# Kernel tuning notes

Measured on AMD Instinct MI355X. Metric: run time of the kernel, lower is better.

Reference implementation:

```python
import jax, jax.numpy as jnp
import numpy as np

HIDDEN = 768
NUM_HEADS = 12
HEAD_DIM = HIDDEN // NUM_HEADS
WINDOW = 128
NEG = -1e30  # stand-in for -inf that is safe under autodiff


def setup_inputs() -> dict:
    key = jax.random.key(0)
    ks = jax.random.split(key, 12)
    B, S = 2, 2048
    hidden = jax.random.normal(ks[0], (B, S, HIDDEN), dtype=jnp.float32)
    attention_mask = jnp.ones((B, S), dtype=jnp.int32)
    global_mask = jax.random.randint(ks[1], (B, S), 0, 2, dtype=jnp.int32)
    def lin(kw, kb):
        W = jax.random.normal(kw, (HIDDEN, HIDDEN), dtype=jnp.float32) * 0.02
        b = jax.random.normal(kb, (HIDDEN,), dtype=jnp.float32) * 0.02
        return W, b
    Wq, bq = lin(ks[2], ks[3])
    Wk, bk = lin(ks[4], ks[5])
    Wv, bv = lin(ks[6], ks[7])
    Wo, bo = lin(ks[8], ks[9])
    return {"hidden": hidden, "attention_mask": attention_mask, "global_mask": global_mask,
            "Wq": Wq, "bq": bq, "Wk": Wk, "bk": bk, "Wv": Wv, "bv": bv, "Wo": Wo, "bo": bo}


def _attend(hidden, attention_mask, global_mask, Wq, bq, Wk, bk, Wv, bv, Wo, bo):
    B, S, H = hidden.shape
    def proj(W, b):
        # (B,S,H) -> (B,nh,S,hd); nn.Linear computes x @ W.T + b
        return (hidden @ W.T + b).reshape(B, S, NUM_HEADS, HEAD_DIM).transpose(0, 2, 1, 3)
    q, k, v = proj(Wq, bq), proj(Wk, bk), proj(Wv, bv)
    scale = jnp.asarray(np.sqrt(HEAD_DIM), dtype=hidden.dtype)
    scores = jnp.einsum('bhqd,bhkd->bhqk', q, k) / scale  # (B,nh,S,S)
    # sliding window mask: |i-j| <= WINDOW
    idx = jnp.arange(S)
    window = (jnp.abs(idx[:, None] - idx[None, :]) <= WINDOW)  # (S,S)
    g = global_mask.astype(bool)
    combined = window[None] | g[:, :, None] | g[:, None, :]     # (B,S,S)
    combined = combined & attention_mask.astype(bool)[:, None, :]  # pad mask on keys
    scores = jnp.where(combined[:, None, :, :], scores, NEG)
    attn = jax.nn.softmax(scores, axis=-1)
    # torch code zeroes NaN rows (fully masked); replicate safely
    attn = jnp.where(jnp.isnan(attn), 0.0, attn)
    out = jnp.einsum('bhqk,bhkd->bhqd', attn, v)  # (B,nh,S,hd)
    out = out.transpose(0, 2, 1, 3).reshape(B, S, H)
    return out @ Wo.T + bo


def reference(hidden, attention_mask, global_mask, Wq, bq, Wk, bk, Wv, bv, Wo, bo):
    return _attend(hidden, attention_mask, global_mask, Wq, bq, Wk, bk, Wv, bv, Wo, bo)
```

## Files before the change

### kernel.cpp

```cpp
#include <hip/hip_runtime.h>
#include <math.h>

#define S_LEN 2048
#define HID   768
#define NH    12
#define HD    64
#define WIN   128
#define NEGV  (-1e30f)
#define QSCALE 0.1803368801111204f
#define MCONST 12.0f
#define NROW  49152

typedef __attribute__((ext_vector_type(8))) short short8v;
typedef __attribute__((ext_vector_type(16))) float f32x16;
typedef unsigned short u16;

__device__ __forceinline__ u16 f2bf(float f) {
    union { float f; unsigned int u; } c; c.f = f;
    unsigned int u = c.u + 0x7FFFu + ((c.u >> 16) & 1u);
    return (u16)(u >> 16);
}

__device__ __forceinline__ short8v cvt8(float4 a, float4 b) {
    short8v t;
    t[0]=(short)f2bf(a.x); t[1]=(short)f2bf(a.y); t[2]=(short)f2bf(a.z); t[3]=(short)f2bf(a.w);
    t[4]=(short)f2bf(b.x); t[5]=(short)f2bf(b.y); t[6]=(short)f2bf(b.z); t[7]=(short)f2bf(b.w);
    return t;
}

__device__ __forceinline__ unsigned int pk2bf(float a, float b) {
    unsigned int r;
    asm("v_cvt_pk_bf16_f32 %0, %1, %2" : "=v"(r) : "v"(a), "v"(b));
    return r;
}

__device__ __forceinline__ float exp2_fast(float x) {
    float r;
    asm("v_exp_f32 %0, %1" : "=v"(r) : "v"(x));
    return r;
}

__device__ __forceinline__ float bf2f(u16 v) {
    union { float f; unsigned u; } c; c.u = ((unsigned)v) << 16; return c.f;
}

__device__ __forceinline__ void gload_lds16(const void* g, void* l) {
    __builtin_amdgcn_global_load_lds(
        (const __attribute__((address_space(1))) unsigned int*)g,
        (__attribute__((address_space(3))) unsigned int*)l, 16, 0, 0);
}

__device__ __forceinline__ void cinit_uni(f32x16& S, const float* src) {
    #pragma unroll
    for (int m = 0; m < 4; m++) {
        float4 f = *(const float4*)(src + 8*m);
        S[4*m+0]=f.x; S[4*m+1]=f.y; S[4*m+2]=f.z; S[4*m+3]=f.w;
    }
}
__device__ __forceinline__ void cinit_mixed(f32x16& S, const float* fa, const float* fb,
                                            int ebase, int gq) {
    #pragma unroll
    for (int m = 0; m < 4; m++) {
        float4 a = *(const float4*)(fa + 8*m);
        float4 b = *(const float4*)(fb + 8*m);
        const int e = ebase - 8*m;
        S[4*m+0] = (gq || (unsigned)(e     + 128) <= 256u) ? a.x : b.x;
        S[4*m+1] = (gq || (unsigned)(e - 1 + 128) <= 256u) ? a.y : b.y;
        S[4*m+2] = (gq || (unsigned)(e - 2 + 128) <= 256u) ? a.z : b.z;
        S[4*m+3] = (gq || (unsigned)(e - 3 + 128) <= 256u) ? a.w : b.w;
    }
}

__global__ __launch_bounds__(256) void convert_inputs(
    const float* __restrict__ hidden, const float* __restrict__ Wq,
    const float* __restrict__ Wk, const float* __restrict__ Wv,
    const float* __restrict__ Wo, const int* __restrict__ amask,
    const int* __restrict__ gmask, u16* __restrict__ hbf,
    u16* __restrict__ w4, float* __restrict__ fAg, float* __restrict__ fBg)
{
    const int y = blockIdx.y;
    if (y == 5) {
        const int idx = (blockIdx.x*256 + threadIdx.x) * 8;
        if (idx >= 2*S_LEN) return;
        #pragma unroll
        for (int u = 0; u < 8; u++) {
            const int am = amask[idx+u], gk = gmask[idx+u];
            fAg[idx+u] = am ? -MCONST : NEGV;
            fBg[idx+u] = (am && gk) ? -MCONST : NEGV;
        }
        return;
    }
    const float* src; u16* dst; int n; float scale = 1.f;
    if (y == 0) { src = hidden; dst = hbf; n = 4096*HID; }
    else {
        src = (y==1) ? Wq : (y==2) ? Wk : (y==3) ? Wv : Wo;
        dst = w4 + (size_t)(y-1)*HID*HID;
        n = HID*HID;
        if (y == 1) scale = QSCALE;
    }
    const int idx = (blockIdx.x*256 + threadIdx.x) * 8;
    if (idx >= n) return;
    float4 f0 = *(const float4*)(src + idx);
    float4 f1 = *(const float4*)(src + idx + 4);
    f0.x*=scale; f0.y*=scale; f0.z*=scale; f0.w*=scale;
    f1.x*=scale; f1.y*=scale; f1.z*=scale; f1.w*=scale;
    *(short8v*)(dst + idx) = cvt8(f0, f1);
}

typedef __attribute__((ext_vector_type(4))) float float4v;
__global__ __launch_bounds__(256) void gemm_mfma(
    const u16* __restrict__ A, const u16* __restrict__ W4,
    const float* __restrict__ bA, const float* __restrict__ bB,
    const float* __restrict__ bC, u16* __restrict__ obf,
    u16* __restrict__ ovt, float* __restrict__ of32, int mode)
{
    __shared__ __align__(16) u16 As[128*32];
    __shared__ __align__(16) u16 Bs[128*32];

    const int tid = threadIdx.x;
    const int w = tid >> 6, l = tid & 63;
    const int lx = l & 15, lg = l >> 4;
    const int wr = w >> 1, wc = w & 1;
    const int m0 = blockIdx.x * 128, n0 = blockIdx.y * 128;
    const int z = (mode == 0) ? blockIdx.z : 3;
    const float* bias = (mode == 1) ? bA : (z == 0 ? bA : (z == 1 ? bB : bC));
    const float bscale = (mode == 0 && z == 0) ? QSCALE : 1.0f;
    const u16* Wp = W4 + (size_t)z * (HID*HID);

    float4v acc[4][4];
    const float4v fz = {0.f,0.f,0.f,0.f};
    #pragma unroll
    for (int i = 0; i < 4; i++)
        #pragma unroll
        for (int j = 0; j < 4; j++) acc[i][j] = fz;

    for (int kt = 0; kt < HID/32; kt++) {
        const int k0 = kt * 32;
        __syncthreads();
        #pragma unroll
        for (int rnd = 0; rnd < 2; rnd++) {
            const int ch  = rnd*256 + w*64 + l;
            const int row = ch >> 2, kc = ch & 3;
            gload_lds16(A  + (size_t)(m0+row)*HID + k0 + kc*8,
                        As + (size_t)(rnd*256 + w*64)*8);
            gload_lds16(Wp + (size_t)(n0+row)*HID + k0 + kc*8,
                        Bs + (size_t)(rnd*256 + w*64)*8);
        }
        __syncthreads();
        short8v af[4], bfr[4];
        #pragma unroll
        for (int i = 0; i < 4; i++) {
            af[i]  = *(const short8v*)(As + (wr*64 + i*16 + lx)*32 + lg*8);
            bfr[i] = *(const short8v*)(Bs + (wc*64 + i*16 + lx)*32 + lg*8);
        }
        #pragma unroll
        for (int i = 0; i < 4; i++)
            #pragma unroll
            for (int j = 0; j < 4; j++)
                acc[i][j] = __builtin_amdgcn_mfma_f32_16x16x32_bf16(af[i], bfr[j], acc[i][j], 0, 0, 0);
    }

    #pragma unroll
    for (int j = 0; j < 4; j++) {
        const int col = n0 + wc*64 + j*16 + lx;
        const float bval = bias[col] * bscale;
        const int hh = col >> 6, d = col & 63;
        #pragma unroll
        for (int i = 0; i < 4; i++) {
            const int rbase = m0 + wr*64 + i*16 + lg*4;
            const int bb = rbase >> 11, s = rbase & 2047;
            const float v0 = acc[i][j][0] + bval;
            const float v1 = acc[i][j][1] + bval;
            const float v2 = acc[i][j][2] + bval;
            const float v3 = acc[i][j][3] + bval;
            if (mode == 1) {
                of32[(size_t)(rbase+0)*HID + col] = v0;
                of32[(size_t)(rbase+1)*HID + col] = v1;
                of32[(size_t)(rbase+2)*HID + col] = v2;
                of32[(size_t)(rbase+3)*HID + col] = v3;
            } else if (z == 2) {
                uint2 ow; ow.x = pk2bf(v0, v1); ow.y = pk2bf(v2, v3);
                *(uint2*)&ovt[(((size_t)bb*NH + hh)*HD + d)*S_LEN + s] = ow;
            } else {
                u16* base = obf + (size_t)z * ((size_t)2*S_LEN*HID);
                base[(((size_t)bb*NH + hh)*S_LEN + s+0)*HD + d] = f2bf(v0);
                base[(((size_t)bb*NH + hh)*S_LEN + s+1)*HD + d] = f2bf(v1);
                base[(((size_t)bb*NH + hh)*S_LEN + s+2)*HD + d] = f2bf(v2);
                base[(((size_t)bb*NH + hh)*S_LEN + s+3)*HD + d] = f2bf(v3);
            }
        }
    }
}

__global__ __launch_bounds__(256, 3) void attn_split(
    const u16* __restrict__ Q, const u16* __restrict__ K,
    const u16* __restrict__ Vt, const float* __restrict__ fAg,
    const float* __restrict__ fBg, const int* __restrict__ gmask,
    u16* __restrict__ O0, u16* __restrict__ O1, float* __restrict__ Lp)
{
    __shared__ __align__(16) u16 KsA[8*64*8], VsA[8*64*8];
    __shared__ __align__(16) u16 KsB[8*64*8], VsB[8*64*8];
    __shared__ __align__(16) u16 Ps[4*2048];

    const int tid = threadIdx.x;
    const int w   = tid >> 6;
    const int l   = tid & 63;
    const int hi  = l >> 5;
    const int ln31 = l & 31;

    const int bid = blockIdx.x;
    const int swz = (bid & 7) * 96 + (bid >> 3);
    const int half = swz & 1;
    const int q0  = ((swz >> 1) & 15) * 128;
    const int hb  = swz >> 5;
    const int h   = hb % NH;
    const int b   = hb / NH;
    const size_t bh = ((size_t)b*NH + h) * S_LEN;

    const int q_glob = q0 + 32*w + ln31;

    short8v aq[4];
    {
        const u16* qp = Q + (bh + q_glob)*HD + 8*hi;
        aq[0] = *(const short8v*)(qp);
        aq[1] = *(const short8v*)(qp + 16);
        aq[2] = *(const short8v*)(qp + 32);
        aq[3] = *(const short8v*)(qp + 48);
    }
    const int gq = gmask[(size_t)b*S_LEN + q_glob];
    const float* fAb_ = fAg + (size_t)b*S_LEN;
    const float* fBb_ = fBg + (size_t)b*S_LEN;
    const float* fPb_ = gq ? fAb_ : fBb_;

    float l_i = 0.f;
    f32x16 oa0, oa1;
    #pragma unroll
    for (int i = 0; i < 16; i++) { oa0[i] = 0.f; oa1[i] = 0.f; }

    const int str = tid >> 2;
    const int stc = tid & 3;
    const int wbase = ((str >> 5)*4 + stc)*512 + (str & 31)*8;
    const u16* Kbase = K + bh * HD;
    const u16* Vbase = Vt + (size_t)(b*NH + h) * HD * S_LEN;
    char* Pb = (char*)(Ps + w*2048);

    uint4 rk0, rk1, rv0, rv1;

#define STAGE_REGS(KT) do {                                                   \
    const int kk0_ = (KT) * 64;                                               \
    const u16* kp_ = Kbase + (size_t)(kk0_ + str)*HD + stc*16;                \
    rk0 = *(const uint4*)(kp_); rk1 = *(const uint4*)(kp_ + 8);               \
    const u16* vp_ = Vbase + (size_t)str*S_LEN + kk0_ + stc*16;               \
    rv0 = *(const uint4*)(vp_); rv1 = *(const uint4*)(vp_ + 8);               \
} while(0)

#define WRITE_LDS(KS, VS) do {                                                \
    *(uint4*)((KS) + wbase)       = rk0;                                      \
    *(uint4*)((KS) + wbase + 256) = rk1;                                      \
    *(uint4*)((VS) + wbase)       = rv0;                                      \
    *(uint4*)((VS) + wbase + 256) = rv1;                                      \
} while(0)

#define COMPUTE(KS, VS, K0) do {                                              \
    f32x16 s0, s1;                                                            \
    const int diff_ = (K0) - q0;                                              \
    if (diff_ == 0 || diff_ == 64) {                                          \
        cinit_uni(s0, fAb_ + (K0) + 4*hi);                                    \
        cinit_uni(s1, fAb_ + (K0) + 32 + 4*hi);                               \
    } else if (diff_ >= 256 || diff_ <= -192) {                               \
        cinit_uni(s0, fPb_ + (K0) + 4*hi);                                    \
        cinit_uni(s1, fPb_ + (K0) + 32 + 4*hi);                               \
    } else {                                                                  \
        cinit_mixed(s0, fAb_ + (K0) + 4*hi, fBb_ + (K0) + 4*hi,               \
                    q_glob - ((K0) + 4*hi), gq);                              \
        cinit_mixed(s1, fAb_ + (K0) + 32 + 4*hi, fBb_ + (K0) + 32 + 4*hi,     \
                    q_glob - ((K0) + 32 + 4*hi), gq);                         \
    }                                                                         \
    __builtin_amdgcn_s_setprio(1);                                            \
    _Pragma("unroll")                                                         \
    for (int dd = 0; dd < 4; dd++) {                                          \
        short8v ak0 = *(const short8v*)((KS) + dd*512 + l*8);                 \
        short8v ak1 = *(const short8v*)((KS) + (4+dd)*512 + l*8);             \
        s0 = __builtin_amdgcn_mfma_f32_32x32x16_bf16(ak0, aq[dd], s0, 0,0,0); \
        s1 = __builtin_amdgcn_mfma_f32_32x32x16_bf16(ak1, aq[dd], s1, 0,0,0); \
    }                                                                         \
    __builtin_amdgcn_s_setprio(0);                                            \
    _Pragma("unroll")                                                         \
    for (int i = 0; i < 16; i++) {                                            \
        s0[i] = exp2_fast(s0[i]);                                             \
        s1[i] = exp2_fast(s1[i]);                                             \
    }                                                                         \
    {                                                                         \
        float a0 = (s0[0]+s0[1]) + (s0[2]+s0[3]);                             \
        float a1 = (s0[4]+s0[5]) + (s0[6]+s0[7]);                             \
        float a2 = (s0[8]+s0[9]) + (s0[10]+s0[11]);                           \
        float a3 = (s0[12]+s0[13]) + (s0[14]+s0[15]);                         \
        float b0 = (s1[0]+s1[1]) + (s1[2]+s1[3]);                             \
        float b1 = (s1[4]+s1[5]) + (s1[6]+s1[7]);                             \
        float b2 = (s1[8]+s1[9]) + (s1[10]+s1[11]);                           \
        float b3 = (s1[12]+s1[13]) + (s1[14]+s1[15]);                         \
        l_i += ((a0+a1)+(a2+a3)) + ((b0+b1)+(b2+b3));                         \
    }                                                                         \
    _Pragma("unroll")                                                         \
    for (int g = 0; g < 4; g++) {                                             \
        uint2 v0, v1;                                                         \
        v0.x = pk2bf(s0[4*g+0], s0[4*g+1]);                                   \
        v0.y = pk2bf(s0[4*g+2], s0[4*g+3]);                                   \
        v1.x = pk2bf(s1[4*g+0], s1[4*g+1]);                                   \
        v1.y = pk2bf(s1[4*g+2], s1[4*g+3]);                                   \
        const int g0_ = g, g1_ = g + 4;                                       \
        *(uint2*)(Pb + (g0_>>1)*1024 + (((g0_&1)<<5) | ln31)*16 + hi*8) = v0; \
        *(uint2*)(Pb + (g1_>>1)*1024 + (((g1_&1)<<5) | ln31)*16 + hi*8) = v1; \
    }                                                                         \
    __builtin_amdgcn_s_setprio(1);                                            \
    _Pragma("unroll")                                                         \
    for (int c = 0; c < 4; c++) {                                             \
        short8v pb  = *(const short8v*)(Pb + c*1024 + l*16);                  \
        short8v av0 = *(const short8v*)((VS) + c*512 + l*8);                  \
        short8v av1 = *(const short8v*)((VS) + (4+c)*512 + l*8);              \
        oa0 = __builtin_amdgcn_mfma_f32_32x32x16_bf16(av0, pb, oa0, 0,0,0);   \
        oa1 = __builtin_amdgcn_mfma_f32_32x32x16_bf16(av1, pb, oa1, 0,0,0);   \
    }                                                                         \
    __builtin_amdgcn_s_setprio(0);                                            \
} while(0)

    const int t0 = half * 16, t1 = t0 + 16;
    STAGE_REGS(t0);
    WRITE_LDS(KsA, VsA);
    __syncthreads();

    for (int kt = t0; kt < t1; kt += 2) {
        STAGE_REGS(kt+1);
        COMPUTE(KsA, VsA, kt*64);
        WRITE_LDS(KsB, VsB);
        __syncthreads();
        {
            const int kn = (kt+2 < t1) ? (kt+2) : (t1-1);
            STAGE_REGS(kn);
        }
        COMPUTE(KsB, VsB, (kt+1)*64);
        WRITE_LDS(KsA, VsA);
        __syncthreads();
    }

#undef STAGE_REGS
#undef WRITE_LDS
#undef COMPUTE

    l_i += __shfl_xor(l_i, 32);
    {
        u16* op = (half ? O1 : O0) + (bh + q_glob)*HD + 4*hi;
        #pragma unroll
        for (int m = 0; m < 4; m++) {
            *(unsigned*)(op + 8*m)          = pk2bf(oa0[4*m],   oa0[4*m+1]);
            *(unsigned*)(op + 8*m + 2)      = pk2bf(oa0[4*m+2], oa0[4*m+3]);
            *(unsigned*)(op + 32 + 8*m)     = pk2bf(oa1[4*m],   oa1[4*m+1]);
            *(unsigned*)(op + 32 + 8*m + 2) = pk2bf(oa1[4*m+2], oa1[4*m+3]);
        }
        if (l < 32) Lp[half*NROW + bh + q_glob] = l_i;
    }
}

__global__ __launch_bounds__(256) void attn_merge(
    const u16* __restrict__ O0, const u16* __restrict__ O1,
    const float* __restrict__ Lp, u16* __restrict__ AO)
{
    const int idx8 = (blockIdx.x*256 + threadIdx.x) * 8;
    const int b   = idx8 / (S_LEN*HID);
    const int rem = idx8 - b*(S_LEN*HID);
    const int s   = rem / HID;
    const int hd  = rem - s*HID;
    const int hh  = hd >> 6;
    const int d0  = hd & 63;
    const int row = (b*NH + hh)*S_LEN + s;

    const float inv = 1.f / (Lp[row] + Lp[NROW + row]);

    const size_t ioff = (size_t)row*HD + d0;
    uint4 a = *(const uint4*)(O0 + ioff);
    uint4 c = *(const uint4*)(O1 + ioff);
    const u16* ap = (const u16*)&a;
    const u16* cp = (const u16*)&c;
    unsigned ow[4];
    #pragma unroll
    for (int j = 0; j < 4; j++) {
        float f0 = (bf2f(ap[2*j])   + bf2f(cp[2*j]))   * inv;
        float f1 = (bf2f(ap[2*j+1]) + bf2f(cp[2*j+1])) * inv;
        ow[j] = pk2bf(f0, f1);
    }
    uint4 o; o.x=ow[0]; o.y=ow[1]; o.z=ow[2]; o.w=ow[3];
    *(uint4*)(AO + idx8) = o;
}

extern "C" void kernel_launch(void* const* d_in, const int* in_sizes, int n_in,
                              void* d_out, int out_size, void* d_ws, size_t ws_size,
                              hipStream_t stream)
{
    const float* hidden = (const float*)d_in[0];
    const int*   amask  = (const int*)d_in[1];
    const int*   gmask  = (const int*)d_in[2];
    const float* Wq = (const float*)d_in[3];
    const float* bq = (const float*)d_in[4];
    const float* Wk = (const float*)d_in[5];
    const float* bk = (const float*)d_in[6];
    const float* Wv = (const float*)d_in[7];
    const float* bv = (const float*)d_in[8];
    const float* Wo = (const float*)d_in[9];
    const float* bo = (const float*)d_in[10];
    float* out = (float*)d_out;

    char* ws = (char*)d_ws;
    const size_t NTOK = (size_t)2 * S_LEN * HID;
    u16* hbf   = (u16*)(ws);
    u16* w4    = (u16*)(ws + 6291456);
    float* Lp  = (float*)(ws + 6291456);
    u16* qkvbf = (u16*)(ws + 11010048);
    float* fAg = (float*)(ws + 23592960);
    float* fBg = (float*)(ws + 23609344);
    u16* vtbf  = (u16*)(ws + 29884416);
    u16* aobf  = (u16*)(ws + 36175872);

    convert_inputs<<<dim3(1536, 6), 256, 0, stream>>>(
        hidden, Wq, Wk, Wv, Wo, amask, gmask, hbf, w4, fAg, fBg);

    gemm_mfma<<<dim3(32, 6, 3), 256, 0, stream>>>(hbf, w4, bq, bk, bv, qkvbf, vtbf, nullptr, 0);

    u16* Qbf = qkvbf;
    u16* Kbf = qkvbf + NTOK;

    attn_split<<<dim3(768), 256, 0, stream>>>(Qbf, Kbf, vtbf, fAg, fBg, gmask,
                                              aobf, hbf, Lp);

    attn_merge<<<dim3(1536), 256, 0, stream>>>(aobf, hbf, Lp, vtbf);

    gemm_mfma<<<dim3(32, 6), 256, 0, stream>>>(vtbf, w4, bo, nullptr, nullptr, nullptr, nullptr, out, 1);
}
```

Baseline: 107.5 us.

## Fuse attention merge into output GEMM and single-buffer attention LDS for occupancy

Drops the separate attn_merge kernel. The output-projection GEMM now reads both partial attention outputs and the row sums directly, normalizes them, and writes bf16 tiles into LDS, which saves one launch and one round-trip through global memory. Separately, attn_split goes from double-buffered to single-buffered K/V LDS with an extra barrier per tile, and the launch-bounds occupancy hint rises from 3 to 5. The fused GEMM swaps asynchronous global-to-LDS loads for synchronous register loads plus conversion on every k-tile, and each output N-block redoes that merge work.

```diff
diff --git a/kernel.cpp b/kernel.cpp
--- a/kernel.cpp
+++ b/kernel.cpp
@@ -112,7 +112,9 @@
     const u16* __restrict__ A, const u16* __restrict__ W4,
     const float* __restrict__ bA, const float* __restrict__ bB,
     const float* __restrict__ bC, u16* __restrict__ obf,
-    u16* __restrict__ ovt, float* __restrict__ of32, int mode)
+    u16* __restrict__ ovt, float* __restrict__ of32,
+    const u16* __restrict__ O0m, const u16* __restrict__ O1m,
+    const float* __restrict__ Lpm, int mode)
 {
     __shared__ __align__(16) u16 As[128*32];
     __shared__ __align__(16) u16 Bs[128*32];
@@ -141,8 +143,26 @@
         for (int rnd = 0; rnd < 2; rnd++) {
             const int ch  = rnd*256 + w*64 + l;
             const int row = ch >> 2, kc = ch & 3;
-            gload_lds16(A  + (size_t)(m0+row)*HID + k0 + kc*8,
-                        As + (size_t)(rnd*256 + w*64)*8);
+            if (mode == 1) {
+                const int m  = m0 + row;
+                const int kk = k0 + kc*8;
+                const int bb2 = m >> 11, s2 = m & 2047;
+                const int hh2 = kk >> 6, d2 = kk & 63;
+                const size_t rowO = ((size_t)bb2*NH + hh2)*S_LEN + s2;
+                uint4 a0 = *(const uint4*)(O0m + rowO*HD + d2);
+                uint4 a1 = *(const uint4*)(O1m + rowO*HD + d2);
+                const float inv = 1.f / (Lpm[rowO] + Lpm[rowO + NROW]);
+                const u16* p0 = (const u16*)&a0;
+                const u16* p1 = (const u16*)&a1;
+                short8v mm;
+                #pragma unroll
+                for (int j2 = 0; j2 < 8; j2++)
+                    mm[j2] = (short)f2bf((bf2f(p0[j2]) + bf2f(p1[j2])) * inv);
+                *(short8v*)(As + (size_t)ch*8) = mm;
+            } else {
+                gload_lds16(A + (size_t)(m0+row)*HID + k0 + kc*8,
+                            As + (size_t)(rnd*256 + w*64)*8);
+            }
             gload_lds16(Wp + (size_t)(n0+row)*HID + k0 + kc*8,
                         Bs + (size_t)(rnd*256 + w*64)*8);
         }
@@ -192,14 +212,14 @@
     }
 }
 
-__global__ __launch_bounds__(256, 3) void attn_split(
+__global__ __launch_bounds__(256, 5) void attn_split(
     const u16* __restrict__ Q, const u16* __restrict__ K,
     const u16* __restrict__ Vt, const float* __restrict__ fAg,
     const float* __restrict__ fBg, const int* __restrict__ gmask,
     u16* __restrict__ O0, u16* __restrict__ O1, float* __restrict__ Lp)
 {
-    __shared__ __align__(16) u16 KsA[8*64*8], VsA[8*64*8];
-    __shared__ __align__(16) u16 KsB[8*64*8], VsB[8*64*8];
+    __shared__ __align__(16) u16 Ks[8*64*8];
+    __shared__ __align__(16) u16 Vs[8*64*8];
     __shared__ __align__(16) u16 Ps[4*2048];
 
     const int tid = threadIdx.x;
@@ -254,14 +274,14 @@
     rv0 = *(const uint4*)(vp_); rv1 = *(const uint4*)(vp_ + 8);               \
 } while(0)
 
-#define WRITE_LDS(KS, VS) do {                                                \
-    *(uint4*)((KS) + wbase)       = rk0;                                      \
-    *(uint4*)((KS) + wbase + 256) = rk1;                                      \
-    *(uint4*)((VS) + wbase)       = rv0;                                      \
-    *(uint4*)((VS) + wbase + 256) = rv1;                                      \
+#define WRITE_LDS() do {                                                      \
+    *(uint4*)(Ks + wbase)       = rk0;                                        \
+    *(uint4*)(Ks + wbase + 256) = rk1;                                        \
+    *(uint4*)(Vs + wbase)       = rv0;                                        \
+    *(uint4*)(Vs + wbase + 256) = rv1;                                        \
 } while(0)
 
-#define COMPUTE(KS, VS, K0) do {                                              \
+#define COMPUTE(K0) do {                                                      \
     f32x16 s0, s1;                                                            \
     const int diff_ = (K0) - q0;                                              \
     if (diff_ == 0 || diff_ == 64) {                                          \
@@ -279,8 +299,8 @@
     __builtin_amdgcn_s_setprio(1);                                            \
     _Pragma("unroll")                                                         \
     for (int dd = 0; dd < 4; dd++) {                                          \
-        short8v ak0 = *(const short8v*)((KS) + dd*512 + l*8);                 \
-        short8v ak1 = *(const short8v*)((KS) + (4+dd)*512 + l*8);             \
+        short8v ak0 = *(const short8v*)(Ks + dd*512 + l*8);                   \
+        short8v ak1 = *(const short8v*)(Ks + (4+dd)*512 + l*8);               \
         s0 = __builtin_amdgcn_mfma_f32_32x32x16_bf16(ak0, aq[dd], s0, 0,0,0); \
         s1 = __builtin_amdgcn_mfma_f32_32x32x16_bf16(ak1, aq[dd], s1, 0,0,0); \
     }                                                                         \
@@ -316,8 +336,8 @@
     _Pragma("unroll")                                                         \
     for (int c = 0; c < 4; c++) {                                             \
         short8v pb  = *(const short8v*)(Pb + c*1024 + l*16);                  \
-        short8v av0 = *(const short8v*)((VS) + c*512 + l*8);                  \
-        short8v av1 = *(const short8v*)((VS) + (4+c)*512 + l*8);              \
+        short8v av0 = *(const short8v*)(Vs + c*512 + l*8);                    \
+        short8v av1 = *(const short8v*)(Vs + (4+c)*512 + l*8);                \
         oa0 = __builtin_amdgcn_mfma_f32_32x32x16_bf16(av0, pb, oa0, 0,0,0);   \
         oa1 = __builtin_amdgcn_mfma_f32_32x32x16_bf16(av1, pb, oa1, 0,0,0);   \
     }                                                                         \
@@ -326,20 +346,15 @@
 
     const int t0 = half * 16, t1 = t0 + 16;
     STAGE_REGS(t0);
-    WRITE_LDS(KsA, VsA);
+    WRITE_LDS();
     __syncthreads();
 
-    for (int kt = t0; kt < t1; kt += 2) {
-        STAGE_REGS(kt+1);
-        COMPUTE(KsA, VsA, kt*64);
-        WRITE_LDS(KsB, VsB);
+    for (int kt = t0; kt < t1; kt++) {
+        const int kn = (kt+1 < t1) ? (kt+1) : kt;
+        STAGE_REGS(kn);
+        COMPUTE(kt*64);
         __syncthreads();
-        {
-            const int kn = (kt+2 < t1) ? (kt+2) : (t1-1);
-            STAGE_REGS(kn);
-        }
-        COMPUTE(KsB, VsB, (kt+1)*64);
-        WRITE_LDS(KsA, VsA);
+        WRITE_LDS();
         __syncthreads();
     }
 
@@ -359,37 +374,6 @@
         }
         if (l < 32) Lp[half*NROW + bh + q_glob] = l_i;
     }
-}
-
-__global__ __launch_bounds__(256) void attn_merge(
-    const u16* __restrict__ O0, const u16* __restrict__ O1,
-    const float* __restrict__ Lp, u16* __restrict__ AO)
-{
-    const int idx8 = (blockIdx.x*256 + threadIdx.x) * 8;
-    const int b   = idx8 / (S_LEN*HID);
-    const int rem = idx8 - b*(S_LEN*HID);
-    const int s   = rem / HID;
-    const int hd  = rem - s*HID;
-    const int hh  = hd >> 6;
-    const int d0  = hd & 63;
-    const int row = (b*NH + hh)*S_LEN + s;
-
-    const float inv = 1.f / (Lp[row] + Lp[NROW + row]);
-
-    const size_t ioff = (size_t)row*HD + d0;
-    uint4 a = *(const uint4*)(O0 + ioff);
-    uint4 c = *(const uint4*)(O1 + ioff);
-    const u16* ap = (const u16*)&a;
-    const u16* cp = (const u16*)&c;
-    unsigned ow[4];
-    #pragma unroll
-    for (int j = 0; j < 4; j++) {
-        float f0 = (bf2f(ap[2*j])   + bf2f(cp[2*j]))   * inv;
-        float f1 = (bf2f(ap[2*j+1]) + bf2f(cp[2*j+1])) * inv;
-        ow[j] = pk2bf(f0, f1);
-    }
-    uint4 o; o.x=ow[0]; o.y=ow[1]; o.z=ow[2]; o.w=ow[3];
-    *(uint4*)(AO + idx8) = o;
 }
 
 extern "C" void kernel_launch(void* const* d_in, const int* in_sizes, int n_in,
@@ -423,7 +407,8 @@
     convert_inputs<<<dim3(1536, 6), 256, 0, stream>>>(
         hidden, Wq, Wk, Wv, Wo, amask, gmask, hbf, w4, fAg, fBg);
 
-    gemm_mfma<<<dim3(32, 6, 3), 256, 0, stream>>>(hbf, w4, bq, bk, bv, qkvbf, vtbf, nullptr, 0);
+    gemm_mfma<<<dim3(32, 6, 3), 256, 0, stream>>>(
+        hbf, w4, bq, bk, bv, qkvbf, vtbf, nullptr, nullptr, nullptr, nullptr, 0);
 
     u16* Qbf = qkvbf;
     u16* Kbf = qkvbf + NTOK;
@@ -431,7 +416,7 @@
     attn_split<<<dim3(768), 256, 0, stream>>>(Qbf, Kbf, vtbf, fAg, fBg, gmask,
                                               aobf, hbf, Lp);
 
-    attn_merge<<<dim3(1536), 256, 0, stream>>>(aobf, hbf, Lp, vtbf);
-
-    gemm_mfma<<<dim3(32, 6), 256, 0, stream>>>(vtbf, w4, bo, nullptr, nullptr, nullptr, nullptr, out, 1);
-}
+    gemm_mfma<<<dim3(32, 6), 256, 0, stream>>>(
+        nullptr, w4, bo, nullptr, nullptr, nullptr, nullptr, out,
+        aobf, hbf, Lp, 1);
+}
```

New measurement: 162.6 us. 51.2% more time.
